# Kernel optimization log

Hardware: AMD Instinct MI355X
Metric: run time of the kernel (lower is better)

Reference implementation:

```python
import jax, jax.numpy as jnp
import numpy as np

EPS_BN = 1e-5
NEG_SLOPE = 0.2

def gat_layer(x, src, dst, N, W, a_src, a_dst, b, heads, ch, concat):
    # x: [N, Fin]; W: [Fin, heads*ch]; a_src/a_dst: [heads, ch]; b: [heads*ch] or [ch]
    xw = (x @ W).reshape(N, heads, ch)                      # [N,H,C]
    al_src = jnp.einsum('nhc,hc->nh', xw, a_src)            # [N,H]
    al_dst = jnp.einsum('nhc,hc->nh', xw, a_dst)
    e = jax.nn.leaky_relu(al_src[src] + al_dst[dst], NEG_SLOPE)  # [E,H]
    m = jax.ops.segment_max(e, dst, num_segments=N)         # segment softmax (stable)
    ee = jnp.exp(e - m[dst])
    s = jax.ops.segment_sum(ee, dst, num_segments=N)
    alpha = ee / (s[dst] + 1e-16)                            # [E,H]
    msg = xw[src] * alpha[:, :, None]                        # [E,H,C]
    out = jax.ops.segment_sum(msg, dst, num_segments=N)      # [N,H,C]
    if concat:
        return out.reshape(N, heads * ch) + b
    return out.mean(axis=1) + b

def setup_inputs():
    key = jax.random.key(0)
    ks = jax.random.split(key, 24)
    N, E, dim_in, dim_out = 20000, 320000, 256, 16
    x = jax.random.normal(ks[0], (N, dim_in), dtype=jnp.float32)
    edge_index = jax.random.randint(ks[1], (2, E), 0, N, dtype=jnp.int64)
    def glorot(k, shape):
        fan = shape[0] + shape[-1]
        return jax.random.uniform(k, shape, jnp.float32, -1.0, 1.0) * np.sqrt(6.0 / fan)
    return {
        'x': x, 'edge_index': edge_index,
        'bn_gamma': jnp.ones((dim_in,), jnp.float32),
        'bn_beta': jnp.zeros((dim_in,), jnp.float32),
        'W1': glorot(ks[2], (dim_in, 16 * 64)),
        'a1_src': glorot(ks[3], (16, 64)), 'a1_dst': glorot(ks[4], (16, 64)),
        'b1': jnp.zeros((16 * 64,), jnp.float32),
        'p1': jnp.float32(0.25),
        'W2': glorot(ks[5], (dim_in + 16 * 64, 8 * 8)),
        'a2_src': glorot(ks[6], (8, 8)), 'a2_dst': glorot(ks[7], (8, 8)),
        'b2': jnp.zeros((8 * 8,), jnp.float32),
        'p2': jnp.float32(0.25),
        'W3': glorot(ks[8], (8 * 8, 8 * dim_out)),
        'a3_src': glorot(ks[9], (8, dim_out)), 'a3_dst': glorot(ks[10], (8, dim_out)),
        'b3': jnp.zeros((dim_out,), jnp.float32),
    }

def reference(x, edge_index, bn_gamma, bn_beta, W1, a1_src, a1_dst, b1, p1,
              W2, a2_src, a2_dst, b2, p2, W3, a3_src, a3_dst, b3):
    N = x.shape[0]
    # PyG GATConv default add_self_loops=True
    loops = jnp.arange(N, dtype=edge_index.dtype)
    src = jnp.concatenate([edge_index[0], loops])
    dst = jnp.concatenate([edge_index[1], loops])
    # BatchNorm1d (training-mode batch stats)
    mu = x.mean(axis=0)
    var = x.var(axis=0)
    x_in = (x - mu) * jax.lax.rsqrt(var + EPS_BN) * bn_gamma + bn_beta
    h = gat_layer(x_in, src, dst, N, W1, a1_src, a1_dst, b1, 16, 64, True)
    h = jnp.where(h >= 0, h, p1 * h)  # PReLU
    h = gat_layer(jnp.concatenate([x_in, h], axis=1), src, dst, N, W2, a2_src, a2_dst, b2, 8, 8, True)
    h = jnp.where(h >= 0, h, p2 * h)
    h = gat_layer(h, src, dst, N, W3, a3_src, a3_dst, b3, 8, b3.shape[0], False)
    return jax.nn.log_softmax(h, axis=1)
```

## Files before the change

### kernel.cpp

```cpp
#include <hip/hip_runtime.h>
#include <math.h>

typedef unsigned int u32;
typedef unsigned short u16;
typedef u32 u32x4 __attribute__((ext_vector_type(4)));
typedef float f32x4 __attribute__((ext_vector_type(4)));

__device__ __forceinline__ u16 f2bf(float f) {
  u32 u = __builtin_bit_cast(u32, f);
  return (u16)((u + 0x7FFFu + ((u >> 16) & 1u)) >> 16);
}
__device__ __forceinline__ float bf2f(u32 lo16) {
  return __builtin_bit_cast(float, lo16 << 16);
}
__device__ __forceinline__ void mfma16(f32x4& c, const u32x4& a, const u32x4& b) {
  asm volatile("v_mfma_f32_16x16x32_bf16 %0, %1, %2, %0" : "+v"(c) : "v"(a), "v"(b));
}
__device__ __forceinline__ float lrelu(float e) { return fmaxf(e, 0.2f * e); }

__global__ void bn_stats_kernel(const float* __restrict__ x, float* __restrict__ musum,
                                float* __restrict__ sqsum, int N, int F) {
  int t = threadIdx.x;
  float s = 0.f, s2 = 0.f;
  for (int r = blockIdx.x; r < N; r += gridDim.x) {
    float v = x[(size_t)r * F + t];
    s += v;
    s2 += v * v;
  }
  atomicAdd(&musum[t], s);
  atomicAdd(&sqsum[t], s2);
}

__global__ void bn_apply_bf16_kernel(const float* __restrict__ x, const float* __restrict__ musum,
                                     const float* __restrict__ sqsum,
                                     const float* __restrict__ gamma,
                                     const float* __restrict__ beta, u16* __restrict__ xin,
                                     int N, float invN) {
  int t = threadIdx.x;
  float mu = musum[t] * invN;
  float var = sqsum[t] * invN - mu * mu;
  float sc = gamma[t] * rsqrtf(var + 1e-5f);
  float sh = beta[t] - mu * sc;
  for (int r = blockIdx.x; r < N; r += gridDim.x) {
    size_t idx = (size_t)r * 256 + t;
    xin[idx] = f2bf(x[idx] * sc + sh);
  }
}

__global__ void csr_count_kernel(const int* __restrict__ ei, int E, int N, int* __restrict__ cnt) {
  int e = blockIdx.x * blockDim.x + threadIdx.x;
  int ET = E + N;
  if (e < ET) {
    int d = (e < E) ? ei[E + e] : (e - E);
    atomicAdd(&cnt[d], 1);
  }
}

__global__ __launch_bounds__(1024) void csr_scan_perm_kernel(int* __restrict__ cnt,
                                                             int* __restrict__ row_ptr,
                                                             int* __restrict__ perm, int N) {
  __shared__ int part[1024];
  __shared__ int bins[256];
  __shared__ int bs[256];
  int t = threadIdx.x;
  int chunk = (N + 1023) / 1024;
  int lo = min(t * chunk, N);
  int hi = min(lo + chunk, N);
  if (t < 256) bins[t] = 0;
  __syncthreads();
  int s = 0;
  for (int i = lo; i < hi; i++) {
    int d = cnt[i];
    s += d;
    atomicAdd(&bins[min(d, 255)], 1);
  }
  part[t] = s;
  __syncthreads();
  for (int off = 1; off < 1024; off <<= 1) {
    int v = (t >= off) ? part[t - off] : 0;
    __syncthreads();
    part[t] += v;
    __syncthreads();
  }
  if (t < 256) bs[t] = bins[t];
  __syncthreads();
  for (int off = 1; off < 256; off <<= 1) {
    int v = (t < 256 && t >= off) ? bs[t - off] : 0;
    __syncthreads();
    if (t < 256) bs[t] += v;
    __syncthreads();
  }
  if (t < 256) bins[t] = (t == 0) ? 0 : bs[t - 1];
  __syncthreads();
  for (int i = lo; i < hi; i++) {
    int d = min(cnt[i], 255);
    int pos = atomicAdd(&bins[d], 1);
    perm[pos] = i;
  }
  __syncthreads();
  int run = (t == 0) ? 0 : part[t - 1];
  for (int i = lo; i < hi; i++) {
    int d = cnt[i];
    row_ptr[i] = run;
    cnt[i] = run;
    run += d;
  }
  if (t == 1023) row_ptr[N] = part[1023];
}

__global__ void csr_fill_kernel(const int* __restrict__ ei, int E, int N,
                                int* __restrict__ cursor, int* __restrict__ csr_src) {
  int e = blockIdx.x * blockDim.x + threadIdx.x;
  int ET = E + N;
  if (e < ET) {
    int s, d;
    if (e < E) { s = ei[e]; d = ei[E + e]; }
    else       { s = e - E; d = s; }
    int pos = atomicAdd(&cursor[d], 1);
    csr_src[pos] = s;
  }
}

__global__ void wt_alfold_build(const float* __restrict__ W1, const float* __restrict__ a1s,
                                const float* __restrict__ a1d, const float* __restrict__ W2,
                                const float* __restrict__ a2s, const float* __restrict__ a2d,
                                const float* __restrict__ W3, const float* __restrict__ a3s,
                                const float* __restrict__ a3d, u16* __restrict__ Wt1,
                                u16* __restrict__ Wt2, u16* __restrict__ Wt3) {
  const int S1 = 1024 * 256, S2 = 64 * 1280, S3 = 128 * 64;
  const int A1 = 32 * 256, A2 = 16 * 1280, A3 = 16 * 64;
  const int Z1 = 96 * 256, Z2 = 16 * 1280, Z3 = 16 * 64;
  int idx = blockIdx.x * blockDim.x + threadIdx.x;
  int o = idx;
  if (o < S1) {
    int n = o / 256, k = o % 256;
    Wt1[o] = f2bf(W1[(size_t)k * 1024 + n]);
    return;
  }
  o -= S1;
  if (o < S2) {
    int n = o / 1280, k = o % 1280;
    Wt2[o] = f2bf(W2[(size_t)k * 64 + n]);
    return;
  }
  o -= S2;
  if (o < S3) {
    int n = o / 64, k = o % 64;
    Wt3[o] = f2bf(W3[(size_t)k * 128 + n]);
    return;
  }
  o -= S3;
  if (o < A1) {
    int jj = o / 256, k = o % 256, h = jj >> 1;
    const float* av = (jj & 1) ? a1d : a1s;
    float s = 0.f;
    for (int c = 0; c < 64; c++) s += W1[(size_t)k * 1024 + h * 64 + c] * av[h * 64 + c];
    Wt1[(size_t)(1024 + jj) * 256 + k] = f2bf(s);
    return;
  }
  o -= A1;
  if (o < A2) {
    int jj = o / 1280, k = o % 1280, h = jj >> 1;
    const float* av = (jj & 1) ? a2d : a2s;
    float s = 0.f;
    for (int c = 0; c < 8; c++) s += W2[(size_t)k * 64 + h * 8 + c] * av[h * 8 + c];
    Wt2[(size_t)(64 + jj) * 1280 + k] = f2bf(s);
    return;
  }
  o -= A2;
  if (o < A3) {
    int jj = o / 64, k = o % 64, h = jj >> 1;
    const float* av = (jj & 1) ? a3d : a3s;
    float s = 0.f;
    for (int c = 0; c < 16; c++) s += W3[(size_t)k * 128 + h * 16 + c] * av[h * 16 + c];
    Wt3[(size_t)(128 + jj) * 64 + k] = f2bf(s);
    return;
  }
  o -= A3;
  if (o < Z1) { Wt1[1056 * 256 + o] = 0; return; }
  o -= Z1;
  if (o < Z2) { Wt2[80 * 1280 + o] = 0; return; }
  o -= Z2;
  if (o < Z3) { Wt3[144 * 64 + o] = 0; return; }
}

template <int BM, int BN, int FM, int FN>
__global__ __launch_bounds__(256) void mfma_gemm_al(
    const u16* __restrict__ A1, const u16* __restrict__ A2, int K1, int K,
    const u16* __restrict__ Wt, u16* __restrict__ Ch, int NcH,
    float* __restrict__ als, float* __restrict__ ald, int ALN, int ALP, int M) {
  constexpr int BK = 32;
  constexpr int ACH = (BM * BK) / 8;
  constexpr int BCH = (BN * BK) / 8;
  static_assert(BM == 2 * FM * 16 && BN == 2 * FN * 16, "wave grid 2x2");
  __shared__ u16 As[2][BM * BK];
  __shared__ u16 Bs[2][BN * BK];
  int t = threadIdx.x;
  int m0 = blockIdx.x * BM, n0 = blockIdx.y * BN;
  int r = t & 15;
  int g = (t >> 4) & 3;
  int wid = t >> 6;
  int wm0 = (wid >> 1) * (FM * 16);
  int wn0 = (wid & 1) * (FN * 16);
  int K8 = K >> 3;
  int K2 = K - K1;

  auto stage = [&](int buf, int k0) {
    const u16* Aseg;
    int sA, kl;
    if (k0 < K1) { Aseg = A1; sA = K1; kl = k0; }
    else         { Aseg = A2; sA = K2; kl = k0 - K1; }
#pragma unroll
    for (int i = 0; i < (ACH + 255) / 256; i++) {
      int c = i * 256 + t;
      if (ACH % 256 == 0 || c < ACH) {
        int m = c >> 2, kb = c & 3;
        __builtin_amdgcn_global_load_lds(
            (const __attribute__((address_space(1))) void*)(Aseg + (size_t)(m0 + m) * sA + kl + kb * 8),
            (__attribute__((address_space(3))) void*)(&As[buf][c * 8]), 16, 0, 0);
      }
    }
#pragma unroll
    for (int i = 0; i < (BCH + 255) / 256; i++) {
      int c = i * 256 + t;
      if (BCH % 256 == 0 || c < BCH) {
        int nn = c >> 2, kb = c & 3;
        __builtin_amdgcn_global_load_lds(
            (const __attribute__((address_space(1))) void*)(Wt + ((size_t)(n0 + nn) * K8 + (k0 >> 3) + kb) * 8),
            (__attribute__((address_space(3))) void*)(&Bs[buf][c * 8]), 16, 0, 0);
      }
    }
  };

  f32x4 acc[FM][FN] = {};
  asm volatile("s_nop 7\n\ts_nop 7" :::);

  stage(0, 0);
  __syncthreads();
  int nt = K / BK;
  for (int ts = 0; ts < nt; ts++) {
    if (ts + 1 < nt) stage((ts + 1) & 1, (ts + 1) * BK);
    int cur = ts & 1;
    u32x4 af[FM], bfr[FN];
#pragma unroll
    for (int fi = 0; fi < FM; fi++)
      af[fi] = *(const u32x4*)(&As[cur][((wm0 + fi * 16 + r) * 4 + g) * 8]);
#pragma unroll
    for (int fj = 0; fj < FN; fj++)
      bfr[fj] = *(const u32x4*)(&Bs[cur][((wn0 + fj * 16 + r) * 4 + g) * 8]);
#pragma unroll
    for (int fi = 0; fi < FM; fi++)
#pragma unroll
      for (int fj = 0; fj < FN; fj++) mfma16(acc[fi][fj], af[fi], bfr[fj]);
    __syncthreads();
  }
  asm volatile("s_nop 7\n\ts_nop 7" :::);

#pragma unroll
  for (int fi = 0; fi < FM; fi++) {
#pragma unroll
    for (int fj = 0; fj < FN; fj++) {
#pragma unroll
      for (int v = 0; v < 4; v++) {
        int m = m0 + wm0 + fi * 16 + g * 4 + v;
        int nn = n0 + wn0 + fj * 16 + r;
        if (m < M) {
          float val = acc[fi][fj][v];
          if (nn < NcH) {
            Ch[(size_t)m * NcH + nn] = f2bf(val);
          } else {
            int j = nn - NcH;
            if (j < ALN) ((j & 1) ? ald : als)[(size_t)(j >> 1) * ALP + m] = val;
          }
        }
      }
    }
  }
}

__global__ __launch_bounds__(256) void gat_agg1_gs(
    const u16* __restrict__ xwh, const float* __restrict__ alsrc,
    const float* __restrict__ aldst, const int* __restrict__ row_ptr,
    const int* __restrict__ csr_src, const int* __restrict__ perm,
    const float* __restrict__ bias, const float* __restrict__ slope_p,
    u16* __restrict__ out, int N, int ALP, int NBH) {
  constexpr int U = 6;
  int b = blockIdx.x;
  int xcd = b & 7, seq = b >> 3;
  int phase = seq / NBH, nb = seq - phase * NBH;
  int h = xcd + (phase << 3);
  int lane = threadIdx.x & 63;
  int g = lane >> 3, l8 = lane & 7;
  int ti = nb * 32 + (threadIdx.x >> 6) * 8 + g;
  int n = perm[min(ti, N - 1)];
  const float* alh = alsrc + (size_t)h * ALP;
  float ad = aldst[(size_t)h * ALP + n];
  int start = row_ptr[n];
  int end = row_ptr[n + 1];
  int deg = (ti < N) ? end - start : 0;
  int endm1 = end - 1;

  float m = -1e30f, s = 0.f;
  float acc[8] = {};
  const u16* base = xwh + (size_t)h * 64 + (size_t)l8 * 8;

  auto fma8 = [&](const u32x4& v, float w) {
#pragma unroll
    for (int i = 0; i < 4; i++) {
      u32 u = v[i];
      acc[2 * i] = fmaf(w, bf2f(u & 0xffffu), acc[2 * i]);
      acc[2 * i + 1] = fmaf(w, bf2f(u >> 16), acc[2 * i + 1]);
    }
  };

  int c[U];
#pragma unroll
  for (int i = 0; i < U; i++) c[i] = csr_src[min(start + i, endm1)];
  int j = 0;
  for (; j + U <= deg; j += U) {
    u32x4 v[U];
    float e[U];
#pragma unroll
    for (int i = 0; i < U; i++) v[i] = *(const u32x4*)(base + (size_t)c[i] * 1024);
#pragma unroll
    for (int i = 0; i < U; i++) e[i] = lrelu(alh[c[i]] + ad);
#pragma unroll
    for (int i = 0; i < U; i++) c[i] = csr_src[min(start + j + U + i, endm1)];
    float mn = fmaxf(fmaxf(fmaxf(e[0], e[1]), fmaxf(e[2], e[3])), fmaxf(e[4], e[5]));
    if (mn > m) {
      float sc = __expf(m - mn);
      s *= sc;
#pragma unroll
      for (int k = 0; k < 8; k++) acc[k] *= sc;
      m = mn;
    }
#pragma unroll
    for (int i = 0; i < U; i++) {
      float w = __expf(e[i] - m);
      s += w;
      fma8(v[i], w);
    }
  }
  for (int i = 0; j < deg; j++, i++) {
    u32x4 v = *(const u32x4*)(base + (size_t)c[i] * 1024);
    float e = lrelu(alh[c[i]] + ad);
    if (e > m) {
      float sc = __expf(m - e);
      s *= sc;
#pragma unroll
      for (int k = 0; k < 8; k++) acc[k] *= sc;
      m = e;
    }
    float w = __expf(e - m);
    s += w;
    fma8(v, w);
  }
  float rr = 1.f / (s + 1e-16f);

  if (ti < N) {
    float p = slope_p[0];
    u32 ow[4];
#pragma unroll
    for (int i = 0; i < 4; i++) {
      int cc = h * 64 + l8 * 8 + 2 * i;
      float v0 = acc[2 * i] * rr + bias[cc];
      float v1 = acc[2 * i + 1] * rr + bias[cc + 1];
      v0 = (v0 >= 0.f) ? v0 : p * v0;
      v1 = (v1 >= 0.f) ? v1 : p * v1;
      ow[i] = (u32)f2bf(v0) | ((u32)f2bf(v1) << 16);
    }
    *(u32x4*)(out + (size_t)n * 1024 + h * 64 + l8 * 8) = *(u32x4*)ow;
  }
}

__global__ __launch_bounds__(256) void gat_agg2_gs(
    const u16* __restrict__ xwh, const float* __restrict__ alsrc,
    const float* __restrict__ aldst, const int* __restrict__ row_ptr,
    const int* __restrict__ csr_src, const int* __restrict__ perm,
    const float* __restrict__ bias, const float* __restrict__ slope_p,
    u16* __restrict__ out, int N, int ALP) {
  constexpr int U = 4;
  int lane = threadIdx.x & 63;
  int g = lane >> 3, l8 = lane & 7;
  int ti = blockIdx.x * 32 + (threadIdx.x >> 6) * 8 + g;
  int n = perm[min(ti, N - 1)];
  const float* alh = alsrc + (size_t)l8 * ALP;
  float ad = aldst[(size_t)l8 * ALP + n];
  int start = row_ptr[n];
  int end = row_ptr[n + 1];
  int deg = (ti < N) ? end - start : 0;
  int endm1 = end - 1;

  float m = -1e30f, s = 0.f;
  float acc[8] = {};
  const u16* base = xwh + (size_t)l8 * 8;

  auto fma8 = [&](const u32x4& v, float w) {
#pragma unroll
    for (int i = 0; i < 4; i++) {
      u32 u = v[i];
      acc[2 * i] = fmaf(w, bf2f(u & 0xffffu), acc[2 * i]);
      acc[2 * i + 1] = fmaf(w, bf2f(u >> 16), acc[2 * i + 1]);
    }
  };

  int c[U];
#pragma unroll
  for (int i = 0; i < U; i++) c[i] = csr_src[min(start + i, endm1)];
  int j = 0;
  for (; j + U <= deg; j += U) {
    u32x4 v[U];
    float e[U];
#pragma unroll
    for (int i = 0; i < U; i++) v[i] = *(const u32x4*)(base + (size_t)c[i] * 64);
#pragma unroll
    for (int i = 0; i < U; i++) e[i] = lrelu(alh[c[i]] + ad);
#pragma unroll
    for (int i = 0; i < U; i++) c[i] = csr_src[min(start + j + U + i, endm1)];
    float mn = fmaxf(fmaxf(e[0], e[1]), fmaxf(e[2], e[3]));
    if (mn > m) {
      float sc = __expf(m - mn);
      s *= sc;
#pragma unroll
      for (int k = 0; k < 8; k++) acc[k] *= sc;
      m = mn;
    }
#pragma unroll
    for (int i = 0; i < U; i++) {
      float w = __expf(e[i] - m);
      s += w;
      fma8(v[i], w);
    }
  }
  for (int i = 0; j < deg; j++, i++) {
    u32x4 v = *(const u32x4*)(base + (size_t)c[i] * 64);
    float e = lrelu(alh[c[i]] + ad);
    if (e > m) {
      float sc = __expf(m - e);
      s *= sc;
#pragma unroll
      for (int k = 0; k < 8; k++) acc[k] *= sc;
      m = e;
    }
    float w = __expf(e - m);
    s += w;
    fma8(v, w);
  }
  float rr = 1.f / (s + 1e-16f);

  if (ti < N) {
    float p = slope_p[0];
    u32 ow[4];
#pragma unroll
    for (int i = 0; i < 4; i++) {
      int cc = l8 * 8 + 2 * i;
      float v0 = acc[2 * i] * rr + bias[cc];
      float v1 = acc[2 * i + 1] * rr + bias[cc + 1];
      v0 = (v0 >= 0.f) ? v0 : p * v0;
      v1 = (v1 >= 0.f) ? v1 : p * v1;
      ow[i] = (u32)f2bf(v0) | ((u32)f2bf(v1) << 16);
    }
    *(u32x4*)(out + (size_t)n * 64 + l8 * 8) = *(u32x4*)ow;
  }
}

__global__ __launch_bounds__(256) void gat_agg3_gs(
    const u16* __restrict__ xwh, const float* __restrict__ alsrc,
    const float* __restrict__ aldst, const int* __restrict__ row_ptr,
    const int* __restrict__ csr_src, const int* __restrict__ perm,
    const float* __restrict__ bias, float* __restrict__ out, int N, int ALP) {
  constexpr int U = 4;
  int lane = threadIdx.x & 63;
  int g = lane >> 4, l16 = lane & 15;
  int head = l16 >> 1;
  int ti = blockIdx.x * 16 + (threadIdx.x >> 6) * 4 + g;
  int n = perm[min(ti, N - 1)];
  const float* alh = alsrc + (size_t)head * ALP;
  float ad = aldst[(size_t)head * ALP + n];
  int start = row_ptr[n];
  int end = row_ptr[n + 1];
  int deg = (ti < N) ? end - start : 0;
  int endm1 = end - 1;

  float m = -1e30f, s = 0.f;
  float acc[8] = {};
  const u16* base = xwh + (size_t)l16 * 8;

  auto fma8 = [&](const u32x4& v, float w) {
#pragma unroll
    for (int i = 0; i < 4; i++) {
      u32 u = v[i];
      acc[2 * i] = fmaf(w, bf2f(u & 0xffffu), acc[2 * i]);
      acc[2 * i + 1] = fmaf(w, bf2f(u >> 16), acc[2 * i + 1]);
    }
  };

  int c[U];
#pragma unroll
  for (int i = 0; i < U; i++) c[i] = csr_src[min(start + i, endm1)];
  int j = 0;
  for (; j + U <= deg; j += U) {
    u32x4 v[U];
    float e[U];
#pragma unroll
    for (int i = 0; i < U; i++) v[i] = *(const u32x4*)(base + (size_t)c[i] * 128);
#pragma unroll
    for (int i = 0; i < U; i++) e[i] = lrelu(alh[c[i]] + ad);
#pragma unroll
    for (int i = 0; i < U; i++) c[i] = csr_src[min(start + j + U + i, endm1)];
    float mn = fmaxf(fmaxf(e[0], e[1]), fmaxf(e[2], e[3]));
    if (mn > m) {
      float sc = __expf(m - mn);
      s *= sc;
#pragma unroll
      for (int k = 0; k < 8; k++) acc[k] *= sc;
      m = mn;
    }
#pragma unroll
    for (int i = 0; i < U; i++) {
      float w = __expf(e[i] - m);
      s += w;
      fma8(v[i], w);
    }
  }
  for (int i = 0; j < deg; j++, i++) {
    u32x4 v = *(const u32x4*)(base + (size_t)c[i] * 128);
    float e = lrelu(alh[c[i]] + ad);
    if (e > m) {
      float sc = __expf(m - e);
      s *= sc;
#pragma unroll
      for (int k = 0; k < 8; k++) acc[k] *= sc;
      m = e;
    }
    float w = __expf(e - m);
    s += w;
    fma8(v, w);
  }
  float rr = 1.f / (s + 1e-16f);
#pragma unroll
  for (int k = 0; k < 8; k++) acc[k] *= rr;

#pragma unroll
  for (int st = 2; st <= 8; st <<= 1)
#pragma unroll
    for (int k = 0; k < 8; k++) acc[k] += __shfl_xor(acc[k], st);

  int half = l16 & 1;
  float v8[8];
  float mx = -1e30f;
#pragma unroll
  for (int k = 0; k < 8; k++) {
    v8[k] = acc[k] * 0.125f + bias[half * 8 + k];
    mx = fmaxf(mx, v8[k]);
  }
  mx = fmaxf(mx, __shfl_xor(mx, 1));
  float se = 0.f;
#pragma unroll
  for (int k = 0; k < 8; k++) se += __expf(v8[k] - mx);
  se += __shfl_xor(se, 1);
  float lse = mx + logf(se);
  if (ti < N && l16 < 2) {
    float4 o0 = make_float4(v8[0] - lse, v8[1] - lse, v8[2] - lse, v8[3] - lse);
    float4 o1 = make_float4(v8[4] - lse, v8[5] - lse, v8[6] - lse, v8[7] - lse);
    float* op = out + (size_t)n * 16 + half * 8;
    *(float4*)op = o0;
    *(float4*)(op + 4) = o1;
  }
}

extern "C" void kernel_launch(void* const* d_in, const int* in_sizes, int n_in,
                              void* d_out, int out_size, void* d_ws, size_t ws_size,
                              hipStream_t stream) {
  const float* x        = (const float*)d_in[0];
  const int*   ei       = (const int*)d_in[1];
  const float* bn_gamma = (const float*)d_in[2];
  const float* bn_beta  = (const float*)d_in[3];
  const float* W1       = (const float*)d_in[4];
  const float* a1s      = (const float*)d_in[5];
  const float* a1d      = (const float*)d_in[6];
  const float* b1       = (const float*)d_in[7];
  const float* p1       = (const float*)d_in[8];
  const float* W2       = (const float*)d_in[9];
  const float* a2s      = (const float*)d_in[10];
  const float* a2d      = (const float*)d_in[11];
  const float* b2       = (const float*)d_in[12];
  const float* p2       = (const float*)d_in[13];
  const float* W3       = (const float*)d_in[14];
  const float* a3s      = (const float*)d_in[15];
  const float* a3d      = (const float*)d_in[16];
  const float* b3       = (const float*)d_in[17];
  float* out = (float*)d_out;

  const int F  = in_sizes[2];
  const int N  = in_sizes[0] / F;
  const int E  = in_sizes[1] / 2;
  const int ET = E + N;
  const int MP = ((N + 127) / 128) * 128;

  size_t off = 0;
  auto alloc = [&](size_t bytes) -> char* {
    char* r = (char*)d_ws + off;
    off += (bytes + 255) & ~(size_t)255;
    return r;
  };
  float* musum   = (float*)alloc(F * 4);
  float* sqsum   = (float*)alloc(F * 4);
  int*   cursor  = (int*)alloc((size_t)N * 4);
  int*   row_ptr = (int*)alloc((size_t)(N + 1) * 4);
  int*   csr_src = (int*)alloc((size_t)ET * 4);
  int*   perm    = (int*)alloc((size_t)N * 4);
  float* al_s    = (float*)alloc((size_t)16 * MP * 4);
  float* al_d    = (float*)alloc((size_t)16 * MP * 4);
  u16*   Wt1     = (u16*)alloc((size_t)1152 * 256 * 2);
  u16*   Wt2     = (u16*)alloc((size_t)96 * 1280 * 2);
  u16*   Wt3     = (u16*)alloc((size_t)160 * 64 * 2);
  u16*   x_in_h  = (u16*)alloc((size_t)MP * 256 * 2);
  u16*   xw1h    = (u16*)alloc((size_t)MP * 1024 * 2);
  u16*   h1      = (u16*)alloc((size_t)MP * 1024 * 2);
  u16*   xw2h    = (u16*)alloc((size_t)MP * 64 * 2);
  u16*   h2h     = (u16*)alloc((size_t)MP * 64 * 2);
  u16*   xw3h    = (u16*)alloc((size_t)MP * 128 * 2);

  hipMemsetAsync(musum, 0, (size_t)2 * F * 4 + (size_t)N * 4, stream);

  bn_stats_kernel<<<256, 256, 0, stream>>>(x, musum, sqsum, N, F);
  bn_apply_bf16_kernel<<<1024, 256, 0, stream>>>(x, musum, sqsum, bn_gamma, bn_beta, x_in_h, N,
                                                 1.0f / (float)N);

  csr_count_kernel<<<(ET + 255) / 256, 256, 0, stream>>>(ei, E, N, cursor);
  csr_scan_perm_kernel<<<1, 1024, 0, stream>>>(cursor, row_ptr, perm, N);
  csr_fill_kernel<<<(ET + 255) / 256, 256, 0, stream>>>(ei, E, N, cursor, csr_src);

  {
    int total = 1024 * 256 + 64 * 1280 + 128 * 64
              + 32 * 256 + 16 * 1280 + 16 * 64
              + 96 * 256 + 16 * 1280 + 16 * 64;
    wt_alfold_build<<<(total + 255) / 256, 256, 0, stream>>>(W1, a1s, a1d, W2, a2s, a2d, W3, a3s,
                                                             a3d, Wt1, Wt2, Wt3);
  }

  {
    dim3 grid(MP / 128, 9);
    mfma_gemm_al<128, 128, 4, 4><<<grid, 256, 0, stream>>>(
        x_in_h, x_in_h, 256, 256, Wt1, xw1h, 1024, al_s, al_d, 32, MP, N);
    int NBH = (N + 31) / 32;
    gat_agg1_gs<<<8 * NBH * 2, 256, 0, stream>>>(xw1h, al_s, al_d, row_ptr, csr_src, perm, b1, p1,
                                                 h1, N, MP, NBH);
  }

  {
    dim3 grid((N + 63) / 64, 1);
    mfma_gemm_al<64, 96, 2, 3><<<grid, 256, 0, stream>>>(
        x_in_h, h1, 256, 1280, Wt2, xw2h, 64, al_s, al_d, 16, MP, N);
    gat_agg2_gs<<<(N + 31) / 32, 256, 0, stream>>>(xw2h, al_s, al_d, row_ptr, csr_src, perm, b2,
                                                   p2, h2h, N, MP);
  }

  {
    dim3 grid((N + 63) / 64, 1);
    mfma_gemm_al<64, 160, 2, 5><<<grid, 256, 0, stream>>>(
        h2h, h2h, 64, 64, Wt3, xw3h, 128, al_s, al_d, 16, MP, N);
    gat_agg3_gs<<<(N + 15) / 16, 256, 0, stream>>>(xw3h, al_s, al_d, row_ptr, csr_src, perm, b3,
                                                   out, N, MP);
  }
}
```

Measured before the change: 313.1 us.

## Merge six preprocessing kernels into three and shrink layer-1 gather unroll

```diff
diff --git a/kernel.cpp b/kernel.cpp
--- a/kernel.cpp
+++ b/kernel.cpp
@@ -18,120 +18,121 @@
 }
 __device__ __forceinline__ float lrelu(float e) { return fmaxf(e, 0.2f * e); }
 
-__global__ void bn_stats_kernel(const float* __restrict__ x, float* __restrict__ musum,
-                                float* __restrict__ sqsum, int N, int F) {
+__global__ void prep1_kernel(const float* __restrict__ x, float* __restrict__ musum,
+                             float* __restrict__ sqsum, const int* __restrict__ ei, int E,
+                             int N, int* __restrict__ cnt) {
+  int b = blockIdx.x;
   int t = threadIdx.x;
-  float s = 0.f, s2 = 0.f;
-  for (int r = blockIdx.x; r < N; r += gridDim.x) {
-    float v = x[(size_t)r * F + t];
-    s += v;
-    s2 += v * v;
-  }
-  atomicAdd(&musum[t], s);
-  atomicAdd(&sqsum[t], s2);
-}
-
-__global__ void bn_apply_bf16_kernel(const float* __restrict__ x, const float* __restrict__ musum,
-                                     const float* __restrict__ sqsum,
-                                     const float* __restrict__ gamma,
-                                     const float* __restrict__ beta, u16* __restrict__ xin,
-                                     int N, float invN) {
+  if (b < 256) {
+    float s = 0.f, s2 = 0.f;
+    for (int r = b; r < N; r += 256) {
+      float v = x[(size_t)r * 256 + t];
+      s += v;
+      s2 += v * v;
+    }
+    atomicAdd(&musum[t], s);
+    atomicAdd(&sqsum[t], s2);
+  } else {
+    int e = (b - 256) * 256 + t;
+    int ET = E + N;
+    if (e < ET) {
+      int d = (e < E) ? ei[E + e] : (e - E);
+      atomicAdd(&cnt[d], 1);
+    }
+  }
+}
+
+__global__ __launch_bounds__(1024) void prep2_kernel(
+    int* __restrict__ cnt, int* __restrict__ row_ptr, int* __restrict__ perm,
+    const float* __restrict__ x, const float* __restrict__ musum,
+    const float* __restrict__ sqsum, const float* __restrict__ gamma,
+    const float* __restrict__ beta, u16* __restrict__ xin, int N, float invN) {
   int t = threadIdx.x;
-  float mu = musum[t] * invN;
-  float var = sqsum[t] * invN - mu * mu;
-  float sc = gamma[t] * rsqrtf(var + 1e-5f);
-  float sh = beta[t] - mu * sc;
-  for (int r = blockIdx.x; r < N; r += gridDim.x) {
-    size_t idx = (size_t)r * 256 + t;
-    xin[idx] = f2bf(x[idx] * sc + sh);
-  }
-}
-
-__global__ void csr_count_kernel(const int* __restrict__ ei, int E, int N, int* __restrict__ cnt) {
-  int e = blockIdx.x * blockDim.x + threadIdx.x;
-  int ET = E + N;
-  if (e < ET) {
-    int d = (e < E) ? ei[E + e] : (e - E);
-    atomicAdd(&cnt[d], 1);
-  }
-}
-
-__global__ __launch_bounds__(1024) void csr_scan_perm_kernel(int* __restrict__ cnt,
-                                                             int* __restrict__ row_ptr,
-                                                             int* __restrict__ perm, int N) {
-  __shared__ int part[1024];
-  __shared__ int bins[256];
-  __shared__ int bs[256];
-  int t = threadIdx.x;
-  int chunk = (N + 1023) / 1024;
-  int lo = min(t * chunk, N);
-  int hi = min(lo + chunk, N);
-  if (t < 256) bins[t] = 0;
-  __syncthreads();
-  int s = 0;
-  for (int i = lo; i < hi; i++) {
-    int d = cnt[i];
-    s += d;
-    atomicAdd(&bins[min(d, 255)], 1);
-  }
-  part[t] = s;
-  __syncthreads();
-  for (int off = 1; off < 1024; off <<= 1) {
-    int v = (t >= off) ? part[t - off] : 0;
+  if (blockIdx.x == 0) {
+    __shared__ int part[1024];
+    __shared__ int bins[256];
+    __shared__ int bs[256];
+    int chunk = (N + 1023) / 1024;
+    int lo = min(t * chunk, N);
+    int hi = min(lo + chunk, N);
+    if (t < 256) bins[t] = 0;
     __syncthreads();
-    part[t] += v;
+    int s = 0;
+    for (int i = lo; i < hi; i++) {
+      int d = cnt[i];
+      s += d;
+      atomicAdd(&bins[min(d, 255)], 1);
+    }
+    part[t] = s;
     __syncthreads();
-  }
-  if (t < 256) bs[t] = bins[t];
-  __syncthreads();
-  for (int off = 1; off < 256; off <<= 1) {
-    int v = (t < 256 && t >= off) ? bs[t - off] : 0;
+    for (int off = 1; off < 1024; off <<= 1) {
+      int v = (t >= off) ? part[t - off] : 0;
+      __syncthreads();
+      part[t] += v;
+      __syncthreads();
+    }
+    if (t < 256) bs[t] = bins[t];
     __syncthreads();
-    if (t < 256) bs[t] += v;
+    for (int off = 1; off < 256; off <<= 1) {
+      int v = (t < 256 && t >= off) ? bs[t - off] : 0;
+      __syncthreads();
+      if (t < 256) bs[t] += v;
+      __syncthreads();
+    }
+    if (t < 256) bins[t] = (t == 0) ? 0 : bs[t - 1];
     __syncthreads();
-  }
-  if (t < 256) bins[t] = (t == 0) ? 0 : bs[t - 1];
-  __syncthreads();
-  for (int i = lo; i < hi; i++) {
-    int d = min(cnt[i], 255);
-    int pos = atomicAdd(&bins[d], 1);
-    perm[pos] = i;
-  }
-  __syncthreads();
-  int run = (t == 0) ? 0 : part[t - 1];
-  for (int i = lo; i < hi; i++) {
-    int d = cnt[i];
-    row_ptr[i] = run;
-    cnt[i] = run;
-    run += d;
-  }
-  if (t == 1023) row_ptr[N] = part[1023];
-}
-
-__global__ void csr_fill_kernel(const int* __restrict__ ei, int E, int N,
-                                int* __restrict__ cursor, int* __restrict__ csr_src) {
-  int e = blockIdx.x * blockDim.x + threadIdx.x;
-  int ET = E + N;
-  if (e < ET) {
-    int s, d;
-    if (e < E) { s = ei[e]; d = ei[E + e]; }
-    else       { s = e - E; d = s; }
-    int pos = atomicAdd(&cursor[d], 1);
-    csr_src[pos] = s;
-  }
-}
-
-__global__ void wt_alfold_build(const float* __restrict__ W1, const float* __restrict__ a1s,
-                                const float* __restrict__ a1d, const float* __restrict__ W2,
-                                const float* __restrict__ a2s, const float* __restrict__ a2d,
-                                const float* __restrict__ W3, const float* __restrict__ a3s,
-                                const float* __restrict__ a3d, u16* __restrict__ Wt1,
-                                u16* __restrict__ Wt2, u16* __restrict__ Wt3) {
+    for (int i = lo; i < hi; i++) {
+      int d = min(cnt[i], 255);
+      int pos = atomicAdd(&bins[d], 1);
+      perm[pos] = i;
+    }
+    __syncthreads();
+    int run = (t == 0) ? 0 : part[t - 1];
+    for (int i = lo; i < hi; i++) {
+      int d = cnt[i];
+      row_ptr[i] = run;
+      cnt[i] = run;
+      run += d;
+    }
+    if (t == 1023) row_ptr[N] = part[1023];
+  } else {
+    int col = t & 255, ro = t >> 8;
+    float mu = musum[col] * invN;
+    float var = sqsum[col] * invN - mu * mu;
+    float sc = gamma[col] * rsqrtf(var + 1e-5f);
+    float sh = beta[col] - mu * sc;
+    for (int r = (blockIdx.x - 1) * 4 + ro; r < N; r += 256 * 4) {
+      size_t idx = (size_t)r * 256 + col;
+      xin[idx] = f2bf(x[idx] * sc + sh);
+    }
+  }
+}
+
+__global__ void prep3_kernel(const int* __restrict__ ei, int E, int N, int FILLB,
+                             int* __restrict__ cursor, int* __restrict__ csr_src,
+                             const float* __restrict__ W1, const float* __restrict__ a1s,
+                             const float* __restrict__ a1d, const float* __restrict__ W2,
+                             const float* __restrict__ a2s, const float* __restrict__ a2d,
+                             const float* __restrict__ W3, const float* __restrict__ a3s,
+                             const float* __restrict__ a3d, u16* __restrict__ Wt1,
+                             u16* __restrict__ Wt2, u16* __restrict__ Wt3) {
+  int b = blockIdx.x;
+  if (b < FILLB) {
+    int e = b * 256 + threadIdx.x;
+    int ET = E + N;
+    if (e < ET) {
+      int s, d;
+      if (e < E) { s = ei[e]; d = ei[E + e]; }
+      else       { s = e - E; d = s; }
+      int pos = atomicAdd(&cursor[d], 1);
+      csr_src[pos] = s;
+    }
+    return;
+  }
   const int S1 = 1024 * 256, S2 = 64 * 1280, S3 = 128 * 64;
   const int A1 = 32 * 256, A2 = 16 * 1280, A3 = 16 * 64;
   const int Z1 = 96 * 256, Z2 = 16 * 1280, Z3 = 16 * 64;
-  int idx = blockIdx.x * blockDim.x + threadIdx.x;
-  int o = idx;
+  int o = (b - FILLB) * 256 + threadIdx.x;
   if (o < S1) {
     int n = o / 256, k = o % 256;
     Wt1[o] = f2bf(W1[(size_t)k * 1024 + n]);
@@ -284,7 +285,7 @@
     const int* __restrict__ csr_src, const int* __restrict__ perm,
     const float* __restrict__ bias, const float* __restrict__ slope_p,
     u16* __restrict__ out, int N, int ALP, int NBH) {
-  constexpr int U = 6;
+  constexpr int U = 4;
   int b = blockIdx.x;
   int xcd = b & 7, seq = b >> 3;
   int phase = seq / NBH, nb = seq - phase * NBH;
@@ -326,7 +327,7 @@
     for (int i = 0; i < U; i++) e[i] = lrelu(alh[c[i]] + ad);
 #pragma unroll
     for (int i = 0; i < U; i++) c[i] = csr_src[min(start + j + U + i, endm1)];
-    float mn = fmaxf(fmaxf(fmaxf(e[0], e[1]), fmaxf(e[2], e[3])), fmaxf(e[4], e[5]));
+    float mn = fmaxf(fmaxf(e[0], e[1]), fmaxf(e[2], e[3]));
     if (mn > m) {
       float sc = __expf(m - mn);
       s *= sc;
@@ -624,20 +625,19 @@
 
   hipMemsetAsync(musum, 0, (size_t)2 * F * 4 + (size_t)N * 4, stream);
 
-  bn_stats_kernel<<<256, 256, 0, stream>>>(x, musum, sqsum, N, F);
-  bn_apply_bf16_kernel<<<1024, 256, 0, stream>>>(x, musum, sqsum, bn_gamma, bn_beta, x_in_h, N,
-                                                 1.0f / (float)N);
-
-  csr_count_kernel<<<(ET + 255) / 256, 256, 0, stream>>>(ei, E, N, cursor);
-  csr_scan_perm_kernel<<<1, 1024, 0, stream>>>(cursor, row_ptr, perm, N);
-  csr_fill_kernel<<<(ET + 255) / 256, 256, 0, stream>>>(ei, E, N, cursor, csr_src);
+  int CNTB = (ET + 255) / 256;
+  prep1_kernel<<<256 + CNTB, 256, 0, stream>>>(x, musum, sqsum, ei, E, N, cursor);
+
+  prep2_kernel<<<257, 1024, 0, stream>>>(cursor, row_ptr, perm, x, musum, sqsum, bn_gamma,
+                                         bn_beta, x_in_h, N, 1.0f / (float)N);
 
   {
-    int total = 1024 * 256 + 64 * 1280 + 128 * 64
-              + 32 * 256 + 16 * 1280 + 16 * 64
-              + 96 * 256 + 16 * 1280 + 16 * 64;
-    wt_alfold_build<<<(total + 255) / 256, 256, 0, stream>>>(W1, a1s, a1d, W2, a2s, a2d, W3, a3s,
-                                                             a3d, Wt1, Wt2, Wt3);
+    int total_wt = 1024 * 256 + 64 * 1280 + 128 * 64
+                 + 32 * 256 + 16 * 1280 + 16 * 64
+                 + 96 * 256 + 16 * 1280 + 16 * 64;
+    int WTB = (total_wt + 255) / 256;
+    prep3_kernel<<<CNTB + WTB, 256, 0, stream>>>(ei, E, N, CNTB, cursor, csr_src, W1, a1s, a1d,
+                                                 W2, a2s, a2d, W3, a3s, a3d, Wt1, Wt2, Wt3);
   }
 
   {
```

After: 307.8 us. Within noise of the previous version (-1.7%).
